# Performance work log

Measured on AMD Instinct MI355X. Metric: run time of the kernel, lower is better.

The kernel has to match this reference:

```python
import jax, jax.numpy as jnp
import numpy as np

B, S, T = 32, 512, 128   # batch, source chars, target (protoform) chars
V, L = 128, 5            # char vocab len(C2I), number of languages
E, H, F = 512, 1024, 2048  # embedding_dim, model_size, feedforward_dim
START_CHAR, SEP_LANG = 1, L - 1


def setup_inputs() -> dict:
    key = jax.random.key(0)
    ks = jax.random.split(key, 32)
    f32 = jnp.float32

    def n(k, shape, fan_in):
        return jax.random.normal(k, shape, dtype=f32) * (1.0 / np.sqrt(fan_in))

    inp = {
        "src_chars": jax.random.randint(ks[0], (B, S), 0, V),
        "src_langs": jax.random.randint(ks[1], (B, S), 0, L),
        "tgt_chars": jax.random.randint(ks[2], (B, T), 0, V),
        # embedding feature extractor
        "char_emb": jax.random.normal(ks[3], (V, E), dtype=f32) * 0.02,
        "lang_emb": jax.random.normal(ks[4], (L, E), dtype=f32) * 0.02,
        "fc_W": n(ks[5], (E, 2 * E), 2 * E),
        "fc_b": jnp.zeros((E,), f32),
        # encoder GRU (PyTorch gate layout r,z,n)
        "enc_Wi": n(ks[6], (3 * H, E), E),
        "enc_Wh": n(ks[7], (3 * H, H), H),
        "enc_bi": jnp.zeros((3 * H,), f32),
        "enc_bh": jnp.zeros((3 * H,), f32),
        # decoder GRU, input = [E ; H]
        "dec_Wi": n(ks[8], (3 * H, E + H), E + H),
        "dec_Wh": n(ks[9], (3 * H, H), H),
        "dec_bi": jnp.zeros((3 * H,), f32),
        "dec_bh": jnp.zeros((3 * H,), f32),
        # attention
        "Wq": n(ks[10], (H, H), H),
        "Wk": n(ks[11], (H, H), H),
        "Wcs": n(ks[12], (H, E), E),
        # MLP H -> 2F -> F -> V
        "W1": n(ks[13], (2 * F, H), H),
        "b1": jnp.zeros((2 * F,), f32),
        "W2": n(ks[14], (F, 2 * F), 2 * F),
        "b2": jnp.zeros((F,), f32),
        "W3": n(ks[15], (V, F), F),
    }
    return inp


def _gru_step(h, x, Wi, Wh, bi, bh):
    gi = x @ Wi.T + bi            # [B, 3H]
    gh = h @ Wh.T + bh            # [B, 3H]
    ir, iz, inn = jnp.split(gi, 3, axis=-1)
    hr, hz, hn = jnp.split(gh, 3, axis=-1)
    r = jax.nn.sigmoid(ir + hr)
    z = jax.nn.sigmoid(iz + hz)
    n = jnp.tanh(inn + r * hn)
    return (1.0 - z) * n + z * h


def _mlp(x, W1, b1, W2, b2, W3):
    h = jax.nn.relu(x @ W1.T + b1)
    h = jax.nn.relu(h @ W2.T + b2)
    return h @ W3.T               # [B, V]


def reference(src_chars, src_langs, tgt_chars,
              char_emb, lang_emb, fc_W, fc_b,
              enc_Wi, enc_Wh, enc_bi, enc_bh,
              dec_Wi, dec_Wh, dec_bi, dec_bh,
              Wq, Wk, Wcs,
              W1, b1, W2, b2, W3):
    # --- feature extraction: concat(char_emb, lang_emb) -> Linear(2E -> E) ---
    def embed(c_idx, l_idx):
        ce = char_emb[c_idx]                       # [..., E]
        le = lang_emb[l_idx]                       # [..., E]
        return jnp.concatenate([ce, le], -1) @ fc_W.T + fc_b

    encoded = embed(src_chars, src_langs)          # [B, S, E]

    # --- encoder GRU over source chars ---
    def enc_step(h, x_t):
        h = _gru_step(h, x_t, enc_Wi, enc_Wh, enc_bi, enc_bh)
        return h, h

    h0 = jnp.zeros((encoded.shape[0], enc_Wh.shape[1]), encoded.dtype)
    _, enc_states = jax.lax.scan(enc_step, h0, jnp.swapaxes(encoded, 0, 1))
    enc_states = jnp.swapaxes(enc_states, 0, 1)    # [B, S, H]

    # precompute attention values: W_c_s(encoded) + W_key(keys)  [B, S, H]
    att_vals = encoded @ Wcs.T + enc_states @ Wk.T

    # --- initial decoder step: <s> embedding + last encoder state ---
    start_emb = embed(jnp.full((encoded.shape[0],), START_CHAR),
                      jnp.full((encoded.shape[0],), SEP_LANG))  # [B, E]
    context0 = enc_states[:, -1]                   # [B, H]
    d0 = jnp.zeros_like(context0)
    dec_h = _gru_step(d0, jnp.concatenate([start_emb, context0], -1),
                      dec_Wi, dec_Wh, dec_bi, dec_bh)

    tgt_emb = embed(tgt_chars, jnp.full_like(tgt_chars, SEP_LANG))  # [B, T, E]

    # --- decode T steps with teacher forcing ---
    def dec_step(carry, x_t):
        h, ctx = carry
        scores_t = _mlp(h + ctx, W1, b1, W2, b2, W3)           # [B, V]
        q = h @ Wq.T                                           # [B, H]
        att = jnp.einsum('bsh,bh->bs', enc_states, q)
        w = jax.nn.softmax(att, axis=-1)
        ctx_new = jnp.einsum('bs,bsh->bh', w, att_vals)        # [B, H]
        h_new = _gru_step(h, jnp.concatenate([x_t, ctx_new], -1),
                          dec_Wi, dec_Wh, dec_bi, dec_bh)
        return (h_new, ctx_new), scores_t

    (_, _), scores = jax.lax.scan(dec_step, (dec_h, context0),
                                  jnp.swapaxes(tgt_emb, 0, 1))
    return jnp.swapaxes(scores, 0, 1)              # [B, T, V]
```

## Files before the change

kernel.cpp:

```cpp
#include <hip/hip_runtime.h>
#include <math.h>


#define Bb 32
#define Ss 512
#define Tt 128
#define Vv 128
#define Hh 1024
#define H3 3072
#define APAD 40

typedef __attribute__((ext_vector_type(8))) short bf16x8;
typedef __attribute__((ext_vector_type(4))) float f32x4;

__device__ inline f32x4 mfma_bf16(bf16x8 a, bf16x8 b, f32x4 c) {
  return __builtin_amdgcn_mfma_f32_16x16x32_bf16(a, b, c, 0, 0, 0);
}
__device__ inline unsigned short f2bf(float f) {
  unsigned u = __builtin_bit_cast(unsigned, f);
  unsigned r = (u + 0x7fffu + ((u >> 16) & 1u)) >> 16;
  return (unsigned short)r;
}
__device__ inline float lof(unsigned u) { return __builtin_bit_cast(float, u << 16); }
__device__ inline float hif(unsigned u) { return __builtin_bit_cast(float, u & 0xffff0000u); }
__device__ inline float bf2f(unsigned short h) {
  return __builtin_bit_cast(float, ((unsigned)h) << 16);
}

#define O_ESBF   0UL
#define O_ESQ    33554432UL
#define O_AVBF   67108864UL
#define O_HCBF   100663296UL
#define O_WHE    109051904UL
#define O_WHD    115343360UL
#define O_WIC    121634816UL
#define O_WKB    127926272UL
#define O_WQT    130023424UL
#define O_W1B    132120576UL
#define O_W2B    140509184UL
#define O_W3B    157286400UL
#define O_XCAT   157810688UL
#define O_EMBFC  160432128UL
#define O_GITAB  161742848UL
#define O_AVTAB  169607168UL
#define O_DGIXT  172228608UL
#define O_GH     173801472UL
#define O_GI     174194688UL
#define O_H      174587904UL
#define O_HBF    174718976UL
#define O_CTX    174784512UL
#define O_CTXBF  174915584UL
#define O_ATTL   174981120UL

__global__ void k_xcat(const float* __restrict__ ce, const float* __restrict__ le,
                       float* __restrict__ xcat) {
  int row = blockIdx.x;
  int l = row >> 7, c = row & 127;
  int i = threadIdx.x * 4;
  float4 v;
  if (i < 512) v = *(const float4*)(ce + c * 512 + i);
  else         v = *(const float4*)(le + l * 512 + (i - 512));
  *(float4*)(xcat + (size_t)row * 1024 + i) = v;
}

__global__ void k_cvt(const float* __restrict__ src, int ld, int lc,
                      unsigned short* __restrict__ dst) {
  size_t i = ((size_t)blockIdx.x * 256 + threadIdx.x) * 8;
  size_t r = i >> lc;
  int c = (int)(i & ((1u << lc) - 1));
  const float* s = src + r * (size_t)ld + c;
  float4 v0 = *(const float4*)s;
  float4 v1 = *(const float4*)(s + 4);
  union { unsigned short us[8]; uint4 u; } o;
  o.us[0] = f2bf(v0.x); o.us[1] = f2bf(v0.y); o.us[2] = f2bf(v0.z); o.us[3] = f2bf(v0.w);
  o.us[4] = f2bf(v1.x); o.us[5] = f2bf(v1.y); o.us[6] = f2bf(v1.z); o.us[7] = f2bf(v1.w);
  *(uint4*)(dst + i) = o.u;
}

__global__ void k_transcvt(const float* __restrict__ in, unsigned short* __restrict__ out) {
  __shared__ float t[32][33];
  int c0 = blockIdx.x * 32, r0 = blockIdx.y * 32;
  int tx = threadIdx.x, ty = threadIdx.y;
  for (int i = ty; i < 32; i += 8)
    t[i][tx] = in[(size_t)(r0 + i) * 1024 + c0 + tx];
  __syncthreads();
  for (int i = ty; i < 32; i += 8)
    out[(size_t)(c0 + i) * 1024 + r0 + tx] = f2bf(t[tx][i]);
}

template <bool BIAS>
__global__ __launch_bounds__(256) void k_gemm(
    const float* __restrict__ A, int lda, const float* __restrict__ W, int ldw,
    const float* __restrict__ bias, float* __restrict__ C, int ldc, int K) {
  __shared__ float As[8][128];
  __shared__ float Ws[8][128];
  int tid = threadIdx.x;
  int n0 = blockIdx.x * 128, m0 = blockIdx.y * 128;
  int tx = tid & 15, ty = tid >> 4;
  int lrow = tid >> 1, lseg = (tid & 1) * 4;
  const float* Ap = A + (size_t)(m0 + lrow) * lda + lseg;
  const float* Wp = W + (size_t)(n0 + lrow) * ldw + lseg;
  float acc[8][8];
#pragma unroll
  for (int i = 0; i < 8; ++i)
#pragma unroll
    for (int j = 0; j < 8; ++j) acc[i][j] = 0.f;
  for (int kt = 0; kt < K; kt += 8) {
    float4 av = *(const float4*)(Ap + kt);
    float4 wv = *(const float4*)(Wp + kt);
    __syncthreads();
    As[lseg + 0][lrow] = av.x; As[lseg + 1][lrow] = av.y;
    As[lseg + 2][lrow] = av.z; As[lseg + 3][lrow] = av.w;
    Ws[lseg + 0][lrow] = wv.x; Ws[lseg + 1][lrow] = wv.y;
    Ws[lseg + 2][lrow] = wv.z; Ws[lseg + 3][lrow] = wv.w;
    __syncthreads();
#pragma unroll
    for (int kk = 0; kk < 8; ++kk) {
      float a[8], b[8];
      *(float4*)(a + 0) = *(const float4*)(&As[kk][ty * 8 + 0]);
      *(float4*)(a + 4) = *(const float4*)(&As[kk][ty * 8 + 4]);
      *(float4*)(b + 0) = *(const float4*)(&Ws[kk][tx * 8 + 0]);
      *(float4*)(b + 4) = *(const float4*)(&Ws[kk][tx * 8 + 4]);
#pragma unroll
      for (int i = 0; i < 8; ++i)
#pragma unroll
        for (int j = 0; j < 8; ++j) acc[i][j] = fmaf(a[i], b[j], acc[i][j]);
    }
  }
#pragma unroll
  for (int i = 0; i < 8; ++i) {
    int r = m0 + ty * 8 + i;
#pragma unroll
    for (int j = 0; j < 8; ++j) {
      int c = n0 + tx * 8 + j;
      float v = acc[i][j];
      if (BIAS) v += bias[c];
      C[(size_t)r * ldc + c] = v;
    }
  }
}

template <int EPI, bool RELU, bool BIAS>
__global__ __launch_bounds__(256) void k_bgemm(
    const unsigned short* __restrict__ A, int lda,
    const unsigned short* __restrict__ W, int ldw,
    const float* __restrict__ bias, void* __restrict__ Cout, int ldc, int K,
    const float* __restrict__ avtab, const int* __restrict__ gl,
    const int* __restrict__ gc) {
  __shared__ unsigned short As[128 * APAD];
  __shared__ unsigned short Bs[128 * APAD];
  int tid = threadIdx.x;
  int n0 = blockIdx.x * 128, m0 = blockIdx.y * 128;
  int w = tid >> 6, l = tid & 63;
  int mw = (w & 1) * 64, nw = (w >> 1) * 64;
  int lrow = tid >> 1, lk = (tid & 1) * 16;
  const unsigned short* Ap = A + (size_t)(m0 + lrow) * lda + lk;
  const unsigned short* Wp = W + (size_t)(n0 + lrow) * ldw + lk;
  int fr = l & 15, fk = (l >> 4) * 8;
  f32x4 acc[4][4];
#pragma unroll
  for (int i = 0; i < 4; ++i)
#pragma unroll
    for (int j = 0; j < 4; ++j) acc[i][j] = (f32x4){0.f, 0.f, 0.f, 0.f};
  for (int kt = 0; kt < K; kt += 32) {
    uint4 a0 = *(const uint4*)(Ap + kt);
    uint4 a1 = *(const uint4*)(Ap + kt + 8);
    uint4 b0 = *(const uint4*)(Wp + kt);
    uint4 b1 = *(const uint4*)(Wp + kt + 8);
    __syncthreads();
    *(uint4*)&As[lrow * APAD + lk] = a0;
    *(uint4*)&As[lrow * APAD + lk + 8] = a1;
    *(uint4*)&Bs[lrow * APAD + lk] = b0;
    *(uint4*)&Bs[lrow * APAD + lk + 8] = b1;
    __syncthreads();
    bf16x8 af[4], bfg[4];
#pragma unroll
    for (int i = 0; i < 4; ++i) af[i] = *(const bf16x8*)&As[(mw + i * 16 + fr) * APAD + fk];
#pragma unroll
    for (int j = 0; j < 4; ++j) bfg[j] = *(const bf16x8*)&Bs[(nw + j * 16 + fr) * APAD + fk];
#pragma unroll
    for (int i = 0; i < 4; ++i)
#pragma unroll
      for (int j = 0; j < 4; ++j) acc[i][j] = mfma_bf16(af[i], bfg[j], acc[i][j]);
  }
#pragma unroll
  for (int i = 0; i < 4; ++i)
#pragma unroll
    for (int j = 0; j < 4; ++j) {
      int col = n0 + nw + j * 16 + fr;
#pragma unroll
      for (int r = 0; r < 4; ++r) {
        int row = m0 + mw + i * 16 + (l >> 4) * 4 + r;
        float v = acc[i][j][r];
        if (BIAS) v += bias[col];
        if (RELU) v = fmaxf(v, 0.f);
        if (EPI == 0) {
          ((unsigned short*)Cout)[(size_t)row * ldc + col] = f2bf(v);
        } else if (EPI == 1) {
          int cl = gl[row] * 128 + gc[row];
          ((unsigned short*)Cout)[(size_t)row * ldc + col] =
              f2bf(v + avtab[(size_t)cl * 1024 + col]);
        } else {
          int tt = row >> 5, bb = row & 31;
          ((float*)Cout)[(size_t)bb * (Tt * Vv) + tt * Vv + col] = v;
        }
      }
    }
}

__global__ __launch_bounds__(256) void k_rec(
    const unsigned short* __restrict__ A, const unsigned short* __restrict__ W,
    float* __restrict__ C, int N, int nrec,
    const unsigned short* __restrict__ esq, const float* __restrict__ h,
    const float* __restrict__ ctx, float* __restrict__ attL,
    unsigned short* __restrict__ hc) {
  __shared__ unsigned short As[32 * 1024];
  int tid = threadIdx.x;
  int id = blockIdx.x;
  if (id < nrec) {
    {
      const uint4* src = (const uint4*)A;
      uint4* dst = (uint4*)As;
#pragma unroll
      for (int i = 0; i < 16; ++i) {
        int c = i * 256 + tid;
        int m = c >> 7, kc = c & 127;
        dst[m * 128 + (kc ^ (m & 7))] = src[c];
      }
    }
    __syncthreads();
    int w = tid >> 6, l = tid & 63;
    int nb = id * 64 + w * 16;
    int fr = l & 15, fk8 = (l >> 4);
    const unsigned short* Wp = W + (size_t)(nb + fr) * 1024 + fk8 * 8;
    const bf16x8* Asv = (const bf16x8*)As;
    f32x4 acc0 = (f32x4){0.f, 0.f, 0.f, 0.f}, acc1 = acc0;
#pragma unroll 8
    for (int kt = 0; kt < 1024; kt += 32) {
      int kc8 = (kt >> 3) + fk8;
      bf16x8 bw = *(const bf16x8*)(Wp + kt);
      bf16x8 a0 = Asv[fr * 128 + (kc8 ^ (fr & 7))];
      bf16x8 a1 = Asv[(fr + 16) * 128 + (kc8 ^ (fr & 7))];
      acc0 = mfma_bf16(a0, bw, acc0);
      acc1 = mfma_bf16(a1, bw, acc1);
    }
    int col = nb + fr;
    int rb = (l >> 4) * 4;
#pragma unroll
    for (int r = 0; r < 4; ++r) {
      C[(size_t)(rb + r) * N + col] = acc0[r];
      C[(size_t)(rb + r + 16) * N + col] = acc1[r];
    }
  } else {
    float* hs = (float*)As;
    int a = id - nrec, b = a >> 3, sc = a & 7;
    for (int i = tid; i < 1024; i += 256) hs[i] = h[b * 1024 + i];
    __syncthreads();
    if (sc < 4) {
      int j = sc * 256 + tid;
      hc[b * 1024 + j] = f2bf(hs[j] + ctx[b * 1024 + j]);
    }
    int sg = tid >> 2, li = tid & 3;
    int s = sc * 64 + sg;
    const unsigned short* ep = esq + (size_t)(b * 512 + s) * 1024;
    float acc = 0.f;
#pragma unroll 4
    for (int i = 0; i < 32; ++i) {
      int k = (i * 4 + li) * 8;
      uint4 e = *(const uint4*)(ep + k);
      float4 h0 = *(const float4*)&hs[k];
      float4 h1 = *(const float4*)&hs[k + 4];
      acc += lof(e.x) * h0.x + hif(e.x) * h0.y + lof(e.y) * h0.z + hif(e.y) * h0.w +
             lof(e.z) * h1.x + hif(e.z) * h1.y + lof(e.w) * h1.z + hif(e.w) * h1.w;
    }
    acc += __shfl_xor(acc, 1);
    acc += __shfl_xor(acc, 2);
    if (li == 0) attL[b * 512 + s] = acc;
  }
}

__global__ void k_gates_enc(const float* __restrict__ gh, const float* __restrict__ gitab,
                            const int* __restrict__ sc, const int* __restrict__ sl,
                            const float* __restrict__ bh, float* __restrict__ h,
                            unsigned short* __restrict__ hbf, unsigned short* __restrict__ esb,
                            int s, int first) {
  int idx = blockIdx.x * 256 + threadIdx.x;
  int b = idx >> 10, j = idx & 1023;
  float ghr = bh[j], ghz = bh[1024 + j], ghn = bh[2048 + j];
  if (!first) {
    const float* g = gh + b * H3 + j;
    ghr += g[0]; ghz += g[1024]; ghn += g[2048];
  }
  int cl = sl[b * Ss + s] * 128 + sc[b * Ss + s];
  const float* gi = gitab + (size_t)cl * H3 + j;
  float r = 1.f / (1.f + expf(-(gi[0] + ghr)));
  float z = 1.f / (1.f + expf(-(gi[1024] + ghz)));
  float n = tanhf(gi[2048] + r * ghn);
  float hold = first ? 0.f : h[idx];
  float hn = (1.f - z) * n + z * hold;
  h[idx] = hn;
  unsigned short hb = f2bf(hn);
  hbf[idx] = hb;
  esb[(size_t)(b * Ss + s) * Hh + j] = hb;
}

__global__ void k_gates_dec(const float* __restrict__ gi, const float* __restrict__ gh,
                            const float* __restrict__ dgixt, const int* __restrict__ tgt,
                            const float* __restrict__ bh, float* __restrict__ h,
                            unsigned short* __restrict__ hbf, int t, int hzero, int usestart) {
  int idx = blockIdx.x * 256 + threadIdx.x;
  int b = idx >> 10, j = idx & 1023;
  const float* gp = gi + b * H3 + j;
  float gir = gp[0], giz = gp[1024], gin = gp[2048];
  float ghr = bh[j], ghz = bh[1024 + j], ghn = bh[2048 + j];
  if (!hzero) {
    const float* g = gh + b * H3 + j;
    ghr += g[0]; ghz += g[1024]; ghn += g[2048];
  }
  int c = usestart ? 1 : tgt[b * Tt + t];
  const float* gx = dgixt + (size_t)c * H3 + j;
  gir += gx[0]; giz += gx[1024]; gin += gx[2048];
  float r = 1.f / (1.f + expf(-(gir + ghr)));
  float z = 1.f / (1.f + expf(-(giz + ghz)));
  float n = tanhf(gin + r * ghn);
  float hold = hzero ? 0.f : h[idx];
  float hn = (1.f - z) * n + z * hold;
  h[idx] = hn;
  hbf[idx] = f2bf(hn);
}

__global__ void k_ctxinit(const float* __restrict__ h, float* __restrict__ ctx,
                          unsigned short* __restrict__ ctxbf) {
  int idx = blockIdx.x * 256 + threadIdx.x;
  float v = h[idx];
  ctx[idx] = v;
  ctxbf[idx] = f2bf(v);
}

__global__ __launch_bounds__(256) void k_ctxsm(const float* __restrict__ attL,
                                               const unsigned short* __restrict__ av,
                                               float* __restrict__ ctx,
                                               unsigned short* __restrict__ ctxbf) {
  int jt = blockIdx.x, b = blockIdx.y;
  __shared__ float w[512];
  __shared__ float wm[4];
  __shared__ float wsm[4];
  __shared__ float red2[128];
  int tid = threadIdx.x;
  float a0 = attL[b * Ss + tid * 2];
  float a1 = attL[b * Ss + tid * 2 + 1];
  float m = fmaxf(a0, a1);
  for (int d = 1; d < 64; d <<= 1) m = fmaxf(m, __shfl_xor(m, d));
  if ((tid & 63) == 0) wm[tid >> 6] = m;
  __syncthreads();
  m = fmaxf(fmaxf(wm[0], wm[1]), fmaxf(wm[2], wm[3]));
  float e0 = expf(a0 - m), e1 = expf(a1 - m);
  w[tid * 2] = e0;
  w[tid * 2 + 1] = e1;
  float ssum = e0 + e1;
  for (int d = 1; d < 64; d <<= 1) ssum += __shfl_xor(ssum, d);
  if ((tid & 63) == 0) wsm[tid >> 6] = ssum;
  __syncthreads();
  float scale = 1.f / (wsm[0] + wsm[1] + wsm[2] + wsm[3]);
  int j = jt * 128 + (tid & 127);
  int sh = tid >> 7;
  const unsigned short* avp = av + (size_t)(b * Ss + sh * 256) * Hh + j;
  float acc = 0.f;
#pragma unroll 16
  for (int s = 0; s < 256; ++s) acc += w[sh * 256 + s] * bf2f(avp[(size_t)s * Hh]);
  if (sh == 1) red2[tid & 127] = acc;
  __syncthreads();
  if (sh == 0) {
    float v = (acc + red2[tid & 127]) * scale;
    ctx[b * Hh + j] = v;
    ctxbf[b * Hh + j] = f2bf(v);
  }
}

extern "C" void kernel_launch(void* const* d_in, const int* in_sizes, int n_in,
                              void* d_out, int out_size, void* d_ws, size_t ws_size,
                              hipStream_t stream) {
  (void)in_sizes; (void)n_in; (void)out_size; (void)ws_size;
  const int*   src_chars = (const int*)d_in[0];
  const int*   src_langs = (const int*)d_in[1];
  const int*   tgt_chars = (const int*)d_in[2];
  const float* char_emb  = (const float*)d_in[3];
  const float* lang_emb  = (const float*)d_in[4];
  const float* fc_W  = (const float*)d_in[5];
  const float* fc_b  = (const float*)d_in[6];
  const float* enc_Wi = (const float*)d_in[7];
  const float* enc_Wh = (const float*)d_in[8];
  const float* enc_bi = (const float*)d_in[9];
  const float* enc_bh = (const float*)d_in[10];
  const float* dec_Wi = (const float*)d_in[11];
  const float* dec_Wh = (const float*)d_in[12];
  const float* dec_bi = (const float*)d_in[13];
  const float* dec_bh = (const float*)d_in[14];
  const float* Wq  = (const float*)d_in[15];
  const float* Wk  = (const float*)d_in[16];
  const float* Wcs = (const float*)d_in[17];
  const float* W1 = (const float*)d_in[18];
  const float* b1 = (const float*)d_in[19];
  const float* W2 = (const float*)d_in[20];
  const float* b2 = (const float*)d_in[21];
  const float* W3 = (const float*)d_in[22];
  float* out = (float*)d_out;

  char* ws = (char*)d_ws;
  unsigned short* esbf  = (unsigned short*)(ws + O_ESBF);
  unsigned short* esq   = (unsigned short*)(ws + O_ESQ);
  unsigned short* avbf  = (unsigned short*)(ws + O_AVBF);
  unsigned short* hcbf  = (unsigned short*)(ws + O_HCBF);
  unsigned short* WheB  = (unsigned short*)(ws + O_WHE);
  unsigned short* WhdB  = (unsigned short*)(ws + O_WHD);
  unsigned short* WicB  = (unsigned short*)(ws + O_WIC);
  unsigned short* WkB   = (unsigned short*)(ws + O_WKB);
  unsigned short* WqTB  = (unsigned short*)(ws + O_WQT);
  unsigned short* W1B   = (unsigned short*)(ws + O_W1B);
  unsigned short* W2B   = (unsigned short*)(ws + O_W2B);
  unsigned short* W3B   = (unsigned short*)(ws + O_W3B);
  float* xcat   = (float*)(ws + O_XCAT);
  float* embfc  = (float*)(ws + O_EMBFC);
  float* gitab  = (float*)(ws + O_GITAB);
  float* avtab  = (float*)(ws + O_AVTAB);
  float* dgixt  = (float*)(ws + O_DGIXT);
  float* ghbuf  = (float*)(ws + O_GH);
  float* gibuf  = (float*)(ws + O_GI);
  float* h      = (float*)(ws + O_H);
  unsigned short* hbf   = (unsigned short*)(ws + O_HBF);
  float* ctx    = (float*)(ws + O_CTX);
  unsigned short* ctxbf = (unsigned short*)(ws + O_CTXBF);
  float* attL   = (float*)(ws + O_ATTL);
  unsigned short* G1 = esq;
  unsigned short* G2 = avbf;

  dim3 blk(256);

  k_xcat<<<640, blk, 0, stream>>>(char_emb, lang_emb, xcat);
  k_gemm<true><<<dim3(4, 5), blk, 0, stream>>>(xcat, 1024, fc_W, 1024, fc_b, embfc, 512, 1024);
  k_gemm<true><<<dim3(24, 5), blk, 0, stream>>>(embfc, 512, enc_Wi, 512, enc_bi, gitab, H3, 512);
  k_gemm<false><<<dim3(8, 5), blk, 0, stream>>>(embfc, 512, Wcs, 512, nullptr, avtab, Hh, 512);
  k_gemm<true><<<dim3(24, 1), blk, 0, stream>>>(embfc + 512 * 512, 512, dec_Wi, 1536, dec_bi,
                                                dgixt, H3, 512);
  k_cvt<<<1536, blk, 0, stream>>>(enc_Wh, 1024, 10, WheB);
  k_cvt<<<1536, blk, 0, stream>>>(dec_Wh, 1024, 10, WhdB);
  k_cvt<<<1536, blk, 0, stream>>>(dec_Wi + 512, 1536, 10, WicB);
  k_cvt<<<512,  blk, 0, stream>>>(Wk, 1024, 10, WkB);
  k_cvt<<<2048, blk, 0, stream>>>(W1, 1024, 10, W1B);
  k_cvt<<<4096, blk, 0, stream>>>(W2, 4096, 12, W2B);
  k_cvt<<<128,  blk, 0, stream>>>(W3, 2048, 11, W3B);
  k_transcvt<<<dim3(32, 32), dim3(32, 8), 0, stream>>>(Wq, WqTB);

  for (int s = 0; s < Ss; ++s) {
    if (s > 0)
      k_rec<<<48, blk, 0, stream>>>(hbf, WheB, ghbuf, H3, 48,
                                    nullptr, nullptr, nullptr, nullptr, nullptr);
    k_gates_enc<<<128, blk, 0, stream>>>(ghbuf, gitab, src_chars, src_langs, enc_bh,
                                         h, hbf, esbf, s, s == 0 ? 1 : 0);
  }

  k_bgemm<0, false, false><<<dim3(8, 128), blk, 0, stream>>>(
      esbf, 1024, WqTB, 1024, nullptr, esq, 1024, 1024, nullptr, nullptr, nullptr);
  k_bgemm<1, false, false><<<dim3(8, 128), blk, 0, stream>>>(
      esbf, 1024, WkB, 1024, nullptr, avbf, 1024, 1024, avtab, src_langs, src_chars);

  k_ctxinit<<<128, blk, 0, stream>>>(h, ctx, ctxbf);
  k_rec<<<48, blk, 0, stream>>>(ctxbf, WicB, gibuf, H3, 48,
                                nullptr, nullptr, nullptr, nullptr, nullptr);
  k_gates_dec<<<128, blk, 0, stream>>>(gibuf, ghbuf, dgixt, tgt_chars, dec_bh,
                                       h, hbf, 0, 1, 1);

  for (int t = 0; t < Tt; ++t) {
    k_rec<<<304, blk, 0, stream>>>(hbf, WhdB, ghbuf, H3, 48,
                                   esq, h, ctx, attL, hcbf + (size_t)t * Bb * Hh);
    if (t == Tt - 1) break;
    k_ctxsm<<<dim3(8, 32), blk, 0, stream>>>(attL, avbf, ctx, ctxbf);
    k_rec<<<48, blk, 0, stream>>>(ctxbf, WicB, gibuf, H3, 48,
                                  nullptr, nullptr, nullptr, nullptr, nullptr);
    k_gates_dec<<<128, blk, 0, stream>>>(gibuf, ghbuf, dgixt, tgt_chars, dec_bh,
                                         h, hbf, t, 0, 0);
  }

  k_bgemm<0, true, true><<<dim3(32, 32), blk, 0, stream>>>(
      hcbf, 1024, W1B, 1024, b1, G1, 4096, 1024, nullptr, nullptr, nullptr);
  k_bgemm<0, true, true><<<dim3(16, 32), blk, 0, stream>>>(
      G1, 4096, W2B, 4096, b2, G2, 2048, 4096, nullptr, nullptr, nullptr);
  k_bgemm<2, false, false><<<dim3(1, 32), blk, 0, stream>>>(
      G2, 2048, W3B, 2048, nullptr, out, 0, 2048, nullptr, nullptr, nullptr);
}
```

Baseline: 9.589 ms.

## Fuse GRU recurrent matmul with gate update into single per-step kernel

Replaces the per-step pair of a recurrent GEMM launch and a separate gate kernel with one k_step kernel that computes the 32x3072 h·Wh product via MFMA and applies the GRU gates in-register, for both encoder and decoder input steps. The encoder ping-pongs between two bf16 hidden buffers so a step can read the previous h while writing the new one, and a precomputed transposed char/lang index table replaces per-step index arithmetic. This removes one launch and the gh/gi round trip through global memory per step. The cost is only 64 small single-wave blocks reading weights straight from global with no LDS staging, which may limit bandwidth use per step.

```diff
diff --git a/kernel.cpp b/kernel.cpp
--- a/kernel.cpp
+++ b/kernel.cpp
@@ -63,6 +63,13 @@
   *(float4*)(xcat + (size_t)row * 1024 + i) = v;
 }
 
+__global__ void k_cltab(const int* __restrict__ sc, const int* __restrict__ sl,
+                        int* __restrict__ cl) {
+  int i = blockIdx.x * 256 + threadIdx.x;
+  int b = i >> 9, s = i & 511;
+  cl[s * 32 + b] = sl[b * Ss + s] * 128 + sc[b * Ss + s];
+}
+
 __global__ void k_cvt(const float* __restrict__ src, int ld, int lc,
                       unsigned short* __restrict__ dst) {
   size_t i = ((size_t)blockIdx.x * 256 + threadIdx.x) * 8;
@@ -208,6 +215,76 @@
     }
 }
 
+template <int MODE>
+__global__ __launch_bounds__(64) void k_step(
+    const unsigned short* __restrict__ Wh,
+    const unsigned short* __restrict__ Abf,
+    const float* __restrict__ gtab,
+    const int* __restrict__ idx,
+    const float* __restrict__ ghb,
+    const float* __restrict__ bh,
+    float* __restrict__ h,
+    unsigned short* __restrict__ hbfW,
+    unsigned short* __restrict__ esb,
+    int s, int flags) {
+  int tid = threadIdx.x;
+  int fr = tid & 15, q = tid >> 4;
+  int j = blockIdx.x * 16 + fr;
+  f32x4 acc[2][3];
+#pragma unroll
+  for (int m = 0; m < 2; ++m)
+#pragma unroll
+    for (int g = 0; g < 3; ++g) acc[m][g] = (f32x4){0.f, 0.f, 0.f, 0.f};
+  if (!(flags & 4)) {
+    const unsigned short* A0 = Abf + fr * 1024 + q * 8;
+    const unsigned short* W0 = Wh + (size_t)j * 1024 + q * 8;
+#pragma unroll 8
+    for (int kt = 0; kt < 1024; kt += 32) {
+      bf16x8 a0 = *(const bf16x8*)(A0 + kt);
+      bf16x8 a1 = *(const bf16x8*)(A0 + 16 * 1024 + kt);
+      bf16x8 b0 = *(const bf16x8*)(W0 + kt);
+      bf16x8 b1 = *(const bf16x8*)(W0 + 1024 * 1024 + kt);
+      bf16x8 b2 = *(const bf16x8*)(W0 + 2048 * 1024 + kt);
+      acc[0][0] = mfma_bf16(a0, b0, acc[0][0]);
+      acc[1][0] = mfma_bf16(a1, b0, acc[1][0]);
+      acc[0][1] = mfma_bf16(a0, b1, acc[0][1]);
+      acc[1][1] = mfma_bf16(a1, b1, acc[1][1]);
+      acc[0][2] = mfma_bf16(a0, b2, acc[0][2]);
+      acc[1][2] = mfma_bf16(a1, b2, acc[1][2]);
+    }
+  }
+  float bhr = bh[j], bhz = bh[1024 + j], bhn = bh[2048 + j];
+#pragma unroll
+  for (int m = 0; m < 2; ++m) {
+#pragma unroll
+    for (int r = 0; r < 4; ++r) {
+      int b = m * 16 + q * 4 + r;
+      int c = (MODE == 0) ? idx[s * 32 + b] : ((flags & 2) ? 1 : idx[b * Tt + s]);
+      const float* gp = gtab + (size_t)c * H3 + j;
+      float gir = gp[0], giz = gp[1024], gin = gp[2048];
+      float ghr = bhr, ghz = bhz, ghn = bhn;
+      if (MODE == 0) {
+        ghr += acc[m][0][r]; ghz += acc[m][1][r]; ghn += acc[m][2][r];
+      } else {
+        gir += acc[m][0][r]; giz += acc[m][1][r]; gin += acc[m][2][r];
+        if (!(flags & 1)) {
+          const float* g = ghb + b * H3 + j;
+          ghr += g[0]; ghz += g[1024]; ghn += g[2048];
+        }
+      }
+      float rg = 1.f / (1.f + expf(-(gir + ghr)));
+      float zg = 1.f / (1.f + expf(-(giz + ghz)));
+      float ng = tanhf(gin + rg * ghn);
+      float hold = (flags & 1) ? 0.f : h[b * 1024 + j];
+      float hn = (1.f - zg) * ng + zg * hold;
+      h[b * 1024 + j] = hn;
+      unsigned short hb = f2bf(hn);
+      hbfW[b * 1024 + j] = hb;
+      if (MODE == 0) esb[((size_t)b * Ss + s) * 1024 + j] = hb;
+    }
+  }
+}
+
 __global__ __launch_bounds__(256) void k_rec(
     const unsigned short* __restrict__ A, const unsigned short* __restrict__ W,
     float* __restrict__ C, int N, int nrec,
@@ -277,56 +354,6 @@
     acc += __shfl_xor(acc, 2);
     if (li == 0) attL[b * 512 + s] = acc;
   }
-}
-
-__global__ void k_gates_enc(const float* __restrict__ gh, const float* __restrict__ gitab,
-                            const int* __restrict__ sc, const int* __restrict__ sl,
-                            const float* __restrict__ bh, float* __restrict__ h,
-                            unsigned short* __restrict__ hbf, unsigned short* __restrict__ esb,
-                            int s, int first) {
-  int idx = blockIdx.x * 256 + threadIdx.x;
-  int b = idx >> 10, j = idx & 1023;
-  float ghr = bh[j], ghz = bh[1024 + j], ghn = bh[2048 + j];
-  if (!first) {
-    const float* g = gh + b * H3 + j;
-    ghr += g[0]; ghz += g[1024]; ghn += g[2048];
-  }
-  int cl = sl[b * Ss + s] * 128 + sc[b * Ss + s];
-  const float* gi = gitab + (size_t)cl * H3 + j;
-  float r = 1.f / (1.f + expf(-(gi[0] + ghr)));
-  float z = 1.f / (1.f + expf(-(gi[1024] + ghz)));
-  float n = tanhf(gi[2048] + r * ghn);
-  float hold = first ? 0.f : h[idx];
-  float hn = (1.f - z) * n + z * hold;
-  h[idx] = hn;
-  unsigned short hb = f2bf(hn);
-  hbf[idx] = hb;
-  esb[(size_t)(b * Ss + s) * Hh + j] = hb;
-}
-
-__global__ void k_gates_dec(const float* __restrict__ gi, const float* __restrict__ gh,
-                            const float* __restrict__ dgixt, const int* __restrict__ tgt,
-                            const float* __restrict__ bh, float* __restrict__ h,
-                            unsigned short* __restrict__ hbf, int t, int hzero, int usestart) {
-  int idx = blockIdx.x * 256 + threadIdx.x;
-  int b = idx >> 10, j = idx & 1023;
-  const float* gp = gi + b * H3 + j;
-  float gir = gp[0], giz = gp[1024], gin = gp[2048];
-  float ghr = bh[j], ghz = bh[1024 + j], ghn = bh[2048 + j];
-  if (!hzero) {
-    const float* g = gh + b * H3 + j;
-    ghr += g[0]; ghz += g[1024]; ghn += g[2048];
-  }
-  int c = usestart ? 1 : tgt[b * Tt + t];
-  const float* gx = dgixt + (size_t)c * H3 + j;
-  gir += gx[0]; giz += gx[1024]; gin += gx[2048];
-  float r = 1.f / (1.f + expf(-(gir + ghr)));
-  float z = 1.f / (1.f + expf(-(giz + ghz)));
-  float n = tanhf(gin + r * ghn);
-  float hold = hzero ? 0.f : h[idx];
-  float hn = (1.f - z) * n + z * hold;
-  h[idx] = hn;
-  hbf[idx] = f2bf(hn);
 }
 
 __global__ void k_ctxinit(const float* __restrict__ h, float* __restrict__ ctx,
@@ -425,7 +452,6 @@
   float* avtab  = (float*)(ws + O_AVTAB);
   float* dgixt  = (float*)(ws + O_DGIXT);
   float* ghbuf  = (float*)(ws + O_GH);
-  float* gibuf  = (float*)(ws + O_GI);
   float* h      = (float*)(ws + O_H);
   unsigned short* hbf   = (unsigned short*)(ws + O_HBF);
   float* ctx    = (float*)(ws + O_CTX);
@@ -433,10 +459,13 @@
   float* attL   = (float*)(ws + O_ATTL);
   unsigned short* G1 = esq;
   unsigned short* G2 = avbf;
+  int* cltab = (int*)(ws + O_GI);
+  unsigned short* hbf2 = (unsigned short*)(ws + O_GI + 65536);
 
   dim3 blk(256);
 
   k_xcat<<<640, blk, 0, stream>>>(char_emb, lang_emb, xcat);
+  k_cltab<<<64, blk, 0, stream>>>(src_chars, src_langs, cltab);
   k_gemm<true><<<dim3(4, 5), blk, 0, stream>>>(xcat, 1024, fc_W, 1024, fc_b, embfc, 512, 1024);
   k_gemm<true><<<dim3(24, 5), blk, 0, stream>>>(embfc, 512, enc_Wi, 512, enc_bi, gitab, H3, 512);
   k_gemm<false><<<dim3(8, 5), blk, 0, stream>>>(embfc, 512, Wcs, 512, nullptr, avtab, Hh, 512);
@@ -452,11 +481,10 @@
   k_transcvt<<<dim3(32, 32), dim3(32, 8), 0, stream>>>(Wq, WqTB);
 
   for (int s = 0; s < Ss; ++s) {
-    if (s > 0)
-      k_rec<<<48, blk, 0, stream>>>(hbf, WheB, ghbuf, H3, 48,
-                                    nullptr, nullptr, nullptr, nullptr, nullptr);
-    k_gates_enc<<<128, blk, 0, stream>>>(ghbuf, gitab, src_chars, src_langs, enc_bh,
-                                         h, hbf, esbf, s, s == 0 ? 1 : 0);
+    unsigned short* wb = (s & 1) ? hbf2 : hbf;
+    const unsigned short* rb = (s & 1) ? hbf : hbf2;
+    k_step<0><<<64, 64, 0, stream>>>(WheB, rb, gitab, cltab, nullptr, enc_bh,
+                                     h, wb, esbf, s, s == 0 ? 5 : 0);
   }
 
   k_bgemm<0, false, false><<<dim3(8, 128), blk, 0, stream>>>(
@@ -465,20 +493,16 @@
       esbf, 1024, WkB, 1024, nullptr, avbf, 1024, 1024, avtab, src_langs, src_chars);
 
   k_ctxinit<<<128, blk, 0, stream>>>(h, ctx, ctxbf);
-  k_rec<<<48, blk, 0, stream>>>(ctxbf, WicB, gibuf, H3, 48,
-                                nullptr, nullptr, nullptr, nullptr, nullptr);
-  k_gates_dec<<<128, blk, 0, stream>>>(gibuf, ghbuf, dgixt, tgt_chars, dec_bh,
-                                       h, hbf, 0, 1, 1);
+  k_step<1><<<64, 64, 0, stream>>>(WicB, ctxbf, dgixt, tgt_chars, nullptr, dec_bh,
+                                   h, hbf, nullptr, 0, 3);
 
   for (int t = 0; t < Tt; ++t) {
     k_rec<<<304, blk, 0, stream>>>(hbf, WhdB, ghbuf, H3, 48,
                                    esq, h, ctx, attL, hcbf + (size_t)t * Bb * Hh);
     if (t == Tt - 1) break;
     k_ctxsm<<<dim3(8, 32), blk, 0, stream>>>(attL, avbf, ctx, ctxbf);
-    k_rec<<<48, blk, 0, stream>>>(ctxbf, WicB, gibuf, H3, 48,
-                                  nullptr, nullptr, nullptr, nullptr, nullptr);
-    k_gates_dec<<<128, blk, 0, stream>>>(gibuf, ghbuf, dgixt, tgt_chars, dec_bh,
-                                         h, hbf, t, 0, 0);
+    k_step<1><<<64, 64, 0, stream>>>(WicB, ctxbf, dgixt, tgt_chars, ghbuf, dec_bh,
+                                     h, hbf, nullptr, t, 0);
   }
 
   k_bgemm<0, true, true><<<dim3(32, 32), blk, 0, stream>>>(
```

Result: slower. 13.50 ms (+40.7%).
